# Optimization experiments

Hardware: AMD Instinct MI355X
Metric: run time of the kernel (lower is better)

Reference implementation:

```python
import jax, jax.numpy as jnp
import numpy as np

B = 4096      # batch
H = 512       # hidden_size
V = 512       # vocab_size
T = 31        # max_length + 1
D_IN = 14     # linear_in input features


def setup_inputs() -> dict:
    key = jax.random.key(0)
    ks = jax.random.split(key, 6)
    sc = 1.0 / np.sqrt(H).astype(np.float32)
    return {
        "inputs": jax.random.normal(ks[0], (B, D_IN), jnp.float32),
        "W_in": jax.random.normal(ks[1], (H, D_IN), jnp.float32) * (1.0 / np.sqrt(D_IN).astype(np.float32)),
        "b_in": jnp.zeros((H,), jnp.float32),
        "W_ih": jax.random.normal(ks[2], (3 * H, H), jnp.float32) * sc,
        "b_ih": jnp.zeros((3 * H,), jnp.float32),
        "W_hh": jax.random.normal(ks[3], (3 * H, H), jnp.float32) * sc,
        "b_hh": jnp.zeros((3 * H,), jnp.float32),
        "W_out": jax.random.normal(ks[4], (V, H), jnp.float32) * sc,
        "b_out": jnp.zeros((V,), jnp.float32),
    }


def reference(inputs, W_in, b_in, W_ih, b_ih, W_hh, b_hh, W_out, b_out):
    batch = inputs.shape[0]
    x = inputs @ W_in.T + b_in                     # [B,H]
    # Input projection is loop-invariant (same x fed every step in the original)
    gi = x @ W_ih.T + b_ih                         # [B,3H]
    gi_r, gi_z, gi_n = jnp.split(gi, 3, axis=1)

    def step(h, _):
        gh = h @ W_hh.T + b_hh                     # [B,3H]
        gh_r, gh_z, gh_n = jnp.split(gh, 3, axis=1)
        r = jax.nn.sigmoid(gi_r + gh_r)
        z = jax.nn.sigmoid(gi_z + gh_z)
        n = jnp.tanh(gi_n + r * gh_n)
        h_new = (1.0 - z) * n + z * h              # PyTorch GRUCell update
        return h_new, h_new

    h0 = jnp.zeros((batch, W_hh.shape[1]), x.dtype)
    _, hs = jax.lax.scan(step, h0, None, length=T)  # [T,B,H]
    hs = jnp.transpose(hs, (1, 0, 2))               # [B,T,H]
    logits = jnp.einsum('bth,vh->btv', hs, W_out) + b_out  # [B,T,V]
    outputs = jax.nn.softmax(logits, axis=2)
    hidden_flat = hs.reshape(batch, -1)             # [B,T*H]
    return outputs, hidden_flat
```

## Files before the change

kernel.cpp:

```cpp
#include <hip/hip_runtime.h>

#define NTH 15872

typedef __bf16 bf16x8 __attribute__((ext_vector_type(8)));
typedef float  f32x4  __attribute__((ext_vector_type(4)));

__device__ __forceinline__ unsigned short f2bf(float f) {
    unsigned u = __float_as_uint(f);
    u = u + 0x7fffu + ((u >> 16) & 1u);
    return (unsigned short)(u >> 16);
}
__device__ __forceinline__ float sigm(float x)  { return 1.f / (1.f + __expf(-x)); }
__device__ __forceinline__ float tanhf_(float x){ return 2.f / (1.f + __expf(-2.f * x)) - 1.f; }

__device__ __forceinline__ int lds_off(int r, int kb) {
    return r * 64 + ((kb ^ ((r >> 1) & 3)) << 4);
}
__device__ __forceinline__ int4 ldg16(const char* g0, int stride, int kbyte, int c) {
    int r = c >> 2, kb = c & 3;
    return *(const int4*)(g0 + (size_t)r * stride + kbyte + kb * 16);
}
__device__ __forceinline__ void sts16(char* lds, int c, int4 v) {
    int r = c >> 2, kb = c & 3;
    *(int4*)(lds + lds_off(r, kb)) = v;
}
__device__ __forceinline__ bf16x8 ldsfrag(const char* lds, int row, int hi) {
    return *(const bf16x8*)(lds + lds_off(row, hi));
}
__device__ __forceinline__ int4 pack8(const float* p) {
    float4 a = ((const float4*)p)[0], b = ((const float4*)p)[1];
    union { unsigned short us[8]; int4 v; } u;
    u.us[0]=f2bf(a.x); u.us[1]=f2bf(a.y); u.us[2]=f2bf(a.z); u.us[3]=f2bf(a.w);
    u.us[4]=f2bf(b.x); u.us[5]=f2bf(b.y); u.us[6]=f2bf(b.z); u.us[7]=f2bf(b.w);
    return u.v;
}
__device__ __forceinline__ int4 ldg16_f32(const float* g0, int stride, int koff, int c) {
    int r = c >> 2, kb = c & 3;
    return pack8(g0 + (size_t)r * stride + koff + kb * 8);
}

__global__ __launch_bounds__(256) void k_prep(
    const float* __restrict__ W_ih, const float* __restrict__ W_hh,
    const float* __restrict__ W_out,
    const float* __restrict__ inputs, const float* __restrict__ W_in,
    const float* __restrict__ b_in,
    unsigned short* __restrict__ wih_b,
    unsigned short* __restrict__ Wp,
    unsigned short* __restrict__ wout_b,
    unsigned short* __restrict__ xb) {
    const int bid = blockIdx.x, tid = threadIdx.x;
    if (bid < 768) {
        int i = bid * 256 + tid;
        float4 v = ((const float4*)W_ih)[i];
        ushort4 o; o.x=f2bf(v.x); o.y=f2bf(v.y); o.z=f2bf(v.z); o.w=f2bf(v.w);
        ((ushort4*)wih_b)[i] = o;
    } else if (bid < 1152) {
        int cid = (bid - 768) * 256 + tid;
        int lane = cid & 63, c16 = lane & 15, hi = lane >> 4;
        int wn = (cid >> 6) & 1, nb = (cid >> 7) & 15;
        int v = cid >> 11;
        int kt = v / 3, g = v - kt * 3;
        int row = g * 512 + nb * 32 + wn * 16 + c16;
        ((int4*)Wp)[cid] = pack8(W_hh + (size_t)row * 512 + kt * 32 + hi * 8);
    } else if (bid < 1408) {
        int i = (bid - 1152) * 256 + tid;
        float4 v = ((const float4*)W_out)[i];
        ushort4 o; o.x=f2bf(v.x); o.y=f2bf(v.y); o.z=f2bf(v.z); o.w=f2bf(v.w);
        ((ushort4*)wout_b)[i] = o;
    } else {
        __shared__ float lW[512 * 14];
        __shared__ float lI[8 * 14];
        const int r0 = (bid - 1408) * 8;
#pragma unroll
        for (int i = 0; i < 28; ++i) lW[i * 256 + tid] = W_in[i * 256 + tid];
        if (tid < 112) lI[tid] = inputs[r0 * 14 + tid];
        __syncthreads();
#pragma unroll
        for (int i = 0; i < 16; ++i) {
            int idx = i * 256 + tid, r = idx >> 9, j = idx & 511;
            float acc = b_in[j];
            const float* wr = lW + j * 14;
            const float* ir = lI + r * 14;
#pragma unroll
            for (int k = 0; k < 14; ++k) acc += ir[k] * wr[k];
            xb[(size_t)(r0 + r) * 512 + j] = f2bf(acc);
        }
    }
}

__global__ __launch_bounds__(256) void k_gemm_gi(
    const unsigned short* __restrict__ A,
    const unsigned short* __restrict__ W,
    const float* __restrict__ bias,
    float* __restrict__ C)
{
    __shared__ __align__(16) char lA[128 * 64];
    __shared__ __align__(16) char lB[64 * 64];
    const int tid = threadIdx.x, lane = tid & 63, wid = tid >> 6;
    const int wm = wid >> 1, wn = wid & 1, hi = lane >> 4, c16 = lane & 15;
    const int m0 = blockIdx.x * 128, n0 = blockIdx.y * 64;
    const char* ga = (const char*)(A + (size_t)m0 * 512);
    const char* gb = (const char*)(W + (size_t)n0 * 512);
    f32x4 acc[4][2] = {};
    int4 ra0 = ldg16(ga, 1024, 0, tid);
    int4 ra1 = ldg16(ga, 1024, 0, tid + 256);
    int4 rb0 = ldg16(gb, 1024, 0, tid);
    for (int kt = 0; kt < 16; ++kt) {
        if (kt) __syncthreads();
        sts16(lA, tid, ra0); sts16(lA, tid + 256, ra1); sts16(lB, tid, rb0);
        __syncthreads();
        if (kt < 15) {
            int kb = (kt + 1) * 64;
            ra0 = ldg16(ga, 1024, kb, tid);
            ra1 = ldg16(ga, 1024, kb, tid + 256);
            rb0 = ldg16(gb, 1024, kb, tid);
        }
        bf16x8 af[4];
#pragma unroll
        for (int i = 0; i < 4; ++i) af[i] = ldsfrag(lA, wm * 64 + i * 16 + c16, hi);
#pragma unroll
        for (int j = 0; j < 2; ++j) {
            bf16x8 bfr = ldsfrag(lB, wn * 32 + j * 16 + c16, hi);
#pragma unroll
            for (int i = 0; i < 4; ++i)
                acc[i][j] = __builtin_amdgcn_mfma_f32_16x16x32_bf16(af[i], bfr, acc[i][j], 0, 0, 0);
        }
    }
#pragma unroll
    for (int i = 0; i < 4; ++i) {
        int m = m0 + wm * 64 + i * 16 + hi * 4;
#pragma unroll
        for (int j = 0; j < 2; ++j) {
            int n = n0 + wn * 32 + j * 16 + c16;
            float bj = bias[n];
#pragma unroll
            for (int q = 0; q < 4; ++q)
                C[(size_t)(m + q) * 1536 + n] = acc[i][j][q] + bj;
        }
    }
}

__global__ __launch_bounds__(256) void k_step(
    const unsigned short* __restrict__ Hin, int hstride,
    const unsigned short* __restrict__ Wp,
    const float* __restrict__ gi,
    const float* __restrict__ bhh,
    float* __restrict__ hidden,
    unsigned short* __restrict__ Hout, int ostride,
    int t)
{
    __shared__ __align__(16) char lA[2][64 * 64];
    const int tid = threadIdx.x, lane = tid & 63, wn = tid >> 6;
    const int hi = lane >> 4, c16 = lane & 15;
    const int m0 = blockIdx.x * 64;
    f32x4 acc[3][4] = {};
    if (t > 0) {
        const char* ga = (const char*)(Hin + (size_t)m0 * hstride);
        const int gas = hstride * 2;
        const char* wp = (const char*)Wp + (size_t)(blockIdx.y * 4 + wn) * 1024 + lane * 16;
        int4 ra0 = ldg16(ga, gas, 0, tid);
        bf16x8 Bf[2][3];
#pragma unroll
        for (int g = 0; g < 3; ++g)
            Bf[0][g] = *(const bf16x8*)(wp + (size_t)g * 32768);
        sts16(lA[0], tid, ra0);
        for (int kt = 0; kt < 16; ++kt) {
            const int cur = kt & 1;
            if (kt < 15) {
                int kb = (kt + 1) * 64;
                ra0 = ldg16(ga, gas, kb, tid);
#pragma unroll
                for (int g = 0; g < 3; ++g)
                    Bf[(kt + 1) & 1][g] =
                        *(const bf16x8*)(wp + (size_t)((kt + 1) * 3 + g) * 32768);
            }
            __syncthreads();
            bf16x8 af[4];
#pragma unroll
            for (int i = 0; i < 4; ++i) af[i] = ldsfrag(lA[cur], i * 16 + c16, hi);
#pragma unroll
            for (int g = 0; g < 3; ++g) {
#pragma unroll
                for (int i = 0; i < 4; ++i)
                    acc[g][i] = __builtin_amdgcn_mfma_f32_16x16x32_bf16(af[i], Bf[cur][g], acc[g][i], 0, 0, 0);
            }
            if (kt < 15) sts16(lA[cur ^ 1], tid, ra0);
        }
    }
    const int n = blockIdx.y * 64 + wn * 16 + c16;
    const float br = bhh[n], bz = bhh[512 + n], bn_ = bhh[1024 + n];
#pragma unroll
    for (int i = 0; i < 4; ++i) {
        int mB = m0 + i * 16 + hi * 4;
#pragma unroll
        for (int q = 0; q < 4; ++q) {
            int m = mB + q;
            size_t gb0 = (size_t)m * 1536 + n;
            float pr = gi[gb0]        + acc[0][i][q] + br;
            float pz = gi[gb0 + 512]  + acc[1][i][q] + bz;
            float r  = sigm(pr);
            float z  = sigm(pz);
            float nn = tanhf_(gi[gb0 + 1024] + r * (acc[2][i][q] + bn_));
            float hold = (t > 0) ? hidden[(size_t)m * NTH + (size_t)(t - 1) * 512 + n] : 0.f;
            float hn = (1.f - z) * nn + z * hold;
            hidden[(size_t)m * NTH + (size_t)t * 512 + n] = hn;
            Hout[(size_t)m * ostride + n] = f2bf(hn);
        }
    }
}

template<bool BF16A>
__global__ __launch_bounds__(256) void k_proj(
    const void* __restrict__ Aptr,
    int astr,
    const unsigned short* __restrict__ Wo,
    const float* __restrict__ bo,
    float* __restrict__ out)
{
    __shared__ __align__(16) char lA[64 * 64];
    __shared__ __align__(16) char lB[512 * 64];
    __shared__ float red[2][2][32];
    const int tid = threadIdx.x, lane = tid & 63, wid = tid >> 6;
    const int wm = wid >> 1, wn = wid & 1, hi = lane >> 4, c16 = lane & 15;
    const int m0 = blockIdx.x * 64;
    const char*  gab = (const char*)Aptr  + (size_t)m0 * astr * 2;
    const float* gaf = (const float*)Aptr + (size_t)m0 * astr;
    const char*  gb  = (const char*)Wo;
    f32x4 acc[2][16] = {};
    int4 ra = BF16A ? ldg16(gab, astr * 2, 0, tid) : ldg16_f32(gaf, astr, 0, tid);
    int4 rb[8];
#pragma unroll
    for (int s = 0; s < 8; ++s) rb[s] = ldg16(gb, 1024, 0, tid + 256 * s);
    for (int kt = 0; kt < 16; ++kt) {
        if (kt) __syncthreads();
        sts16(lA, tid, ra);
#pragma unroll
        for (int s = 0; s < 8; ++s) sts16(lB, tid + 256 * s, rb[s]);
        __syncthreads();
        if (kt < 15) {
            ra = BF16A ? ldg16(gab, astr * 2, (kt + 1) * 64, tid)
                       : ldg16_f32(gaf, astr, (kt + 1) * 32, tid);
#pragma unroll
            for (int s = 0; s < 8; ++s) rb[s] = ldg16(gb, 1024, (kt + 1) * 64, tid + 256 * s);
        }
        bf16x8 af[2];
#pragma unroll
        for (int mf = 0; mf < 2; ++mf)
            af[mf] = ldsfrag(lA, wm * 32 + mf * 16 + c16, hi);
#pragma unroll
        for (int nf = 0; nf < 16; ++nf) {
            bf16x8 bfr = ldsfrag(lB, wn * 256 + nf * 16 + c16, hi);
#pragma unroll
            for (int mf = 0; mf < 2; ++mf)
                acc[mf][nf] = __builtin_amdgcn_mfma_f32_16x16x32_bf16(af[mf], bfr, acc[mf][nf], 0, 0, 0);
        }
    }
#pragma unroll
    for (int nf = 0; nf < 16; ++nf) {
        float bj = bo[wn * 256 + nf * 16 + c16];
#pragma unroll
        for (int mf = 0; mf < 2; ++mf)
#pragma unroll
            for (int q = 0; q < 4; ++q)
                acc[mf][nf][q] = __expf(acc[mf][nf][q] + bj);
    }
#pragma unroll
    for (int mf = 0; mf < 2; ++mf)
#pragma unroll
        for (int q = 0; q < 4; ++q) {
            float s = 0.f;
#pragma unroll
            for (int nf = 0; nf < 16; ++nf) s += acc[mf][nf][q];
            s += __shfl_xor(s, 1); s += __shfl_xor(s, 2);
            s += __shfl_xor(s, 4); s += __shfl_xor(s, 8);
            if (c16 == 0) red[wm][wn][mf * 16 + hi * 4 + q] = s;
        }
    __syncthreads();
#pragma unroll
    for (int mf = 0; mf < 2; ++mf)
#pragma unroll
        for (int q = 0; q < 4; ++q) {
            int rl = mf * 16 + hi * 4 + q;
            float inv = 1.f / (red[wm][0][rl] + red[wm][1][rl]);
            int m = m0 + wm * 32 + rl;
            float* orow = out + (size_t)m * 512 + wn * 256 + c16;
#pragma unroll
            for (int nf = 0; nf < 16; ++nf) orow[nf * 16] = acc[mf][nf][q] * inv;
        }
}

extern "C" void kernel_launch(void* const* d_in, const int* in_sizes, int n_in,
                              void* d_out, int out_size, void* d_ws, size_t ws_size,
                              hipStream_t stream) {
    const float* inputs = (const float*)d_in[0];
    const float* W_in   = (const float*)d_in[1];
    const float* b_in   = (const float*)d_in[2];
    const float* W_ih   = (const float*)d_in[3];
    const float* b_ih   = (const float*)d_in[4];
    const float* W_hh   = (const float*)d_in[5];
    const float* b_hh   = (const float*)d_in[6];
    const float* W_out  = (const float*)d_in[7];
    const float* b_out  = (const float*)d_in[8];

    float* out    = (float*)d_out;
    float* hidden = out + (size_t)126976 * 512;

    char* ws = (char*)d_ws;
    unsigned short* wih_b  = (unsigned short*)(ws);
    unsigned short* Wp     = (unsigned short*)(ws + 1572864);
    unsigned short* wout_b = (unsigned short*)(ws + 3145728);
    unsigned short* x_b    = (unsigned short*)(ws + 3670016);
    float*          gi     = (float*)(ws + 7864320);
    const bool big = ws_size >= 163053568ULL;
    unsigned short* hbf2   = (unsigned short*)(ws + 33030144);
    unsigned short* hb0    = (unsigned short*)(ws + 33030144);
    unsigned short* hb1    = (unsigned short*)(ws + 37224448);

    k_prep<<<1920, 256, 0, stream>>>(W_ih, W_hh, W_out, inputs, W_in, b_in,
                                     wih_b, Wp, wout_b, x_b);
    k_gemm_gi<<<dim3(32, 24), 256, 0, stream>>>(x_b, wih_b, b_ih, gi);

    for (int t = 0; t < 31; ++t) {
        const unsigned short* Hin;
        unsigned short* Hout;
        int hs, os;
        if (big) {
            Hin  = hbf2 + (size_t)(t > 0 ? t - 1 : 0) * 512;  hs = NTH;
            Hout = hbf2 + (size_t)t * 512;                     os = NTH;
        } else {
            Hin  = (t & 1) ? hb0 : hb1;  hs = 512;
            Hout = (t & 1) ? hb1 : hb0;  os = 512;
        }
        k_step<<<dim3(64, 8), 256, 0, stream>>>(Hin, hs, Wp, gi, b_hh,
                                                hidden, Hout, os, t);
    }
    if (big) k_proj<true><<<1984, 256, 0, stream>>>(hbf2, 512, wout_b, b_out, out);
    else     k_proj<false><<<1984, 256, 0, stream>>>(hidden, 512, wout_b, b_out, out);
}
```

Baseline: 732.3 us.

## Store hidden state in MFMA fragment layout and load A fragments directly

The step kernel now writes the bf16 hidden state into a pre-packed fragment layout, so the next step can load A operands straight from global memory into registers. This removes the shared-memory staging buffer and the per-iteration __syncthreads. The bf16 history buffer and the bf16 projection path are dropped, so the output projection always reads the fp32 hidden tensor. The trade-off is more redundant global loads across the four waves, and a heavier fp32 read in the final projection.

```diff
diff --git a/kernel.cpp b/kernel.cpp
--- a/kernel.cpp
+++ b/kernel.cpp
@@ -141,60 +141,56 @@
 }
 
 __global__ __launch_bounds__(256) void k_step(
-    const unsigned short* __restrict__ Hin, int hstride,
+    const unsigned short* __restrict__ hPin,
     const unsigned short* __restrict__ Wp,
     const float* __restrict__ gi,
     const float* __restrict__ bhh,
     float* __restrict__ hidden,
-    unsigned short* __restrict__ Hout, int ostride,
+    unsigned short* __restrict__ hPout,
     int t)
 {
-    __shared__ __align__(16) char lA[2][64 * 64];
     const int tid = threadIdx.x, lane = tid & 63, wn = tid >> 6;
     const int hi = lane >> 4, c16 = lane & 15;
-    const int m0 = blockIdx.x * 64;
+    const int bx = blockIdx.x, m0 = bx * 64;
+    const int strip = blockIdx.y * 4 + wn;
     f32x4 acc[3][4] = {};
     if (t > 0) {
-        const char* ga = (const char*)(Hin + (size_t)m0 * hstride);
-        const int gas = hstride * 2;
-        const char* wp = (const char*)Wp + (size_t)(blockIdx.y * 4 + wn) * 1024 + lane * 16;
-        int4 ra0 = ldg16(ga, gas, 0, tid);
-        bf16x8 Bf[2][3];
-#pragma unroll
-        for (int g = 0; g < 3; ++g)
-            Bf[0][g] = *(const bf16x8*)(wp + (size_t)g * 32768);
-        sts16(lA[0], tid, ra0);
+        const char* pa = (const char*)hPin + (size_t)bx * 65536 + lane * 16;
+        const char* wp = (const char*)Wp + (size_t)strip * 1024 + lane * 16;
+        bf16x8 Af[2][4], Bf[2][3];
+#pragma unroll
+        for (int i = 0; i < 4; ++i) Af[0][i] = *(const bf16x8*)(pa + i * 16384);
+#pragma unroll
+        for (int g = 0; g < 3; ++g) Bf[0][g] = *(const bf16x8*)(wp + (size_t)g * 32768);
+#pragma unroll
         for (int kt = 0; kt < 16; ++kt) {
             const int cur = kt & 1;
             if (kt < 15) {
-                int kb = (kt + 1) * 64;
-                ra0 = ldg16(ga, gas, kb, tid);
+#pragma unroll
+                for (int i = 0; i < 4; ++i)
+                    Af[cur ^ 1][i] = *(const bf16x8*)(pa + i * 16384 + (kt + 1) * 1024);
 #pragma unroll
                 for (int g = 0; g < 3; ++g)
-                    Bf[(kt + 1) & 1][g] =
-                        *(const bf16x8*)(wp + (size_t)((kt + 1) * 3 + g) * 32768);
+                    Bf[cur ^ 1][g] = *(const bf16x8*)(wp + (size_t)((kt + 1) * 3 + g) * 32768);
             }
-            __syncthreads();
-            bf16x8 af[4];
-#pragma unroll
-            for (int i = 0; i < 4; ++i) af[i] = ldsfrag(lA[cur], i * 16 + c16, hi);
 #pragma unroll
             for (int g = 0; g < 3; ++g) {
 #pragma unroll
                 for (int i = 0; i < 4; ++i)
-                    acc[g][i] = __builtin_amdgcn_mfma_f32_16x16x32_bf16(af[i], Bf[cur][g], acc[g][i], 0, 0, 0);
+                    acc[g][i] = __builtin_amdgcn_mfma_f32_16x16x32_bf16(Af[cur][i], Bf[cur][g], acc[g][i], 0, 0, 0);
             }
-            if (kt < 15) sts16(lA[cur ^ 1], tid, ra0);
-        }
-    }
-    const int n = blockIdx.y * 64 + wn * 16 + c16;
+        }
+    }
+    const int n = strip * 16 + c16;
+    const int ktn = n >> 5, oct = (n >> 3) & 3, e = n & 7;
     const float br = bhh[n], bz = bhh[512 + n], bn_ = bhh[1024 + n];
 #pragma unroll
     for (int i = 0; i < 4; ++i) {
-        int mB = m0 + i * 16 + hi * 4;
+        const int rb = bx * 4 + i;
+        unsigned short* hc = hPout + ((size_t)(rb * 16 + ktn) << 9) + (oct << 7) + e;
 #pragma unroll
         for (int q = 0; q < 4; ++q) {
-            int m = mB + q;
+            int m = m0 + i * 16 + hi * 4 + q;
             size_t gb0 = (size_t)m * 1536 + n;
             float pr = gi[gb0]        + acc[0][i][q] + br;
             float pz = gi[gb0 + 512]  + acc[1][i][q] + bz;
@@ -204,15 +200,14 @@
             float hold = (t > 0) ? hidden[(size_t)m * NTH + (size_t)(t - 1) * 512 + n] : 0.f;
             float hn = (1.f - z) * nn + z * hold;
             hidden[(size_t)m * NTH + (size_t)t * 512 + n] = hn;
-            Hout[(size_t)m * ostride + n] = f2bf(hn);
+            hc[(size_t)(hi * 4 + q) * 8] = f2bf(hn);
         }
     }
 }
 
 template<bool BF16A>
 __global__ __launch_bounds__(256) void k_proj(
-    const void* __restrict__ Aptr,
-    int astr,
+    const void* __restrict__ Aptr, int astr,
     const unsigned short* __restrict__ Wo,
     const float* __restrict__ bo,
     float* __restrict__ out)
@@ -311,29 +306,18 @@
     unsigned short* wout_b = (unsigned short*)(ws + 3145728);
     unsigned short* x_b    = (unsigned short*)(ws + 3670016);
     float*          gi     = (float*)(ws + 7864320);
-    const bool big = ws_size >= 163053568ULL;
-    unsigned short* hbf2   = (unsigned short*)(ws + 33030144);
-    unsigned short* hb0    = (unsigned short*)(ws + 33030144);
-    unsigned short* hb1    = (unsigned short*)(ws + 37224448);
+    unsigned short* hP0    = (unsigned short*)(ws + 33030144);
+    unsigned short* hP1    = (unsigned short*)(ws + 37224448);
 
     k_prep<<<1920, 256, 0, stream>>>(W_ih, W_hh, W_out, inputs, W_in, b_in,
                                      wih_b, Wp, wout_b, x_b);
     k_gemm_gi<<<dim3(32, 24), 256, 0, stream>>>(x_b, wih_b, b_ih, gi);
 
     for (int t = 0; t < 31; ++t) {
-        const unsigned short* Hin;
-        unsigned short* Hout;
-        int hs, os;
-        if (big) {
-            Hin  = hbf2 + (size_t)(t > 0 ? t - 1 : 0) * 512;  hs = NTH;
-            Hout = hbf2 + (size_t)t * 512;                     os = NTH;
-        } else {
-            Hin  = (t & 1) ? hb0 : hb1;  hs = 512;
-            Hout = (t & 1) ? hb1 : hb0;  os = 512;
-        }
-        k_step<<<dim3(64, 8), 256, 0, stream>>>(Hin, hs, Wp, gi, b_hh,
-                                                hidden, Hout, os, t);
-    }
-    if (big) k_proj<true><<<1984, 256, 0, stream>>>(hbf2, 512, wout_b, b_out, out);
-    else     k_proj<false><<<1984, 256, 0, stream>>>(hidden, 512, wout_b, b_out, out);
-}
+        const unsigned short* hin = (t & 1) ? hP0 : hP1;
+        unsigned short*       hout = (t & 1) ? hP1 : hP0;
+        k_step<<<dim3(64, 8), 256, 0, stream>>>(hin, Wp, gi, b_hh,
+                                                hidden, hout, t);
+    }
+    k_proj<false><<<1984, 256, 0, stream>>>(hidden, 512, wout_b, b_out, out);
+}
```

Result: slower. 873.0 us (+19.2%).
